# Optimization experiments

Measured on AMD Instinct MI355X. Metric: run time of the kernel, lower is better.

The kernel has to match this reference:

```python
import jax, jax.numpy as jnp
import numpy as np

NUM_HEADS = 16
NUM_KV_HEADS = 4
HEAD_DIM = 128
TOP_K = 4
RMS_EPS = 1e-6
ROPE_THETA = 10000.0


def setup_inputs() -> dict:
    key = jax.random.key(0)
    ks = jax.random.split(key, 10)
    T, h, E, I, SI = 1024, 2048, 16, 512, 1024
    s = 0.02  # weight init scale for numerical sanity
    return {
        "hidden_states": jax.random.normal(ks[0], (T, h), jnp.float32),
        "residual": jax.random.normal(ks[1], (T, h), jnp.float32),
        "rms1_w": jnp.ones((h,), jnp.float32),
        "rms2_w": jnp.ones((h,), jnp.float32),
        "w_qkv": jax.random.normal(ks[2], (h, NUM_HEADS * HEAD_DIM + 2 * NUM_KV_HEADS * HEAD_DIM), jnp.float32) * s,
        "w_dense": jax.random.normal(ks[3], (NUM_HEADS * HEAD_DIM, h), jnp.float32) * s,
        "gate_w": jax.random.normal(ks[4], (h, E), jnp.float32) * s,
        "w13": jax.random.normal(ks[5], (E, h, 2 * I), jnp.float32) * s,
        "w2": jax.random.normal(ks[6], (E, I, h), jnp.float32) * s,
        "sw13": jax.random.normal(ks[7], (h, 2 * SI), jnp.float32) * s,
        "sw2": jax.random.normal(ks[8], (SI, h), jnp.float32) * s,
        "position_ids": jnp.arange(T, dtype=jnp.int32),
    }


def _rmsnorm(x, w, eps=RMS_EPS):
    var = jnp.mean(jnp.square(x), axis=-1, keepdims=True)
    return x * jax.lax.rsqrt(var + eps) * w


def _rope_neox(pos, x):
    # x: [T, H, D]; rotate-half (neox) style over full head_dim
    d = x.shape[-1]
    inv_freq = 1.0 / (ROPE_THETA ** (jnp.arange(0, d, 2, dtype=jnp.float32) / d))  # [d/2]
    ang = pos.astype(jnp.float32)[:, None] * inv_freq  # [T, d/2]
    cos = jnp.cos(ang)[:, None, :]  # [T, 1, d/2]
    sin = jnp.sin(ang)[:, None, :]
    x1, x2 = x[..., : d // 2], x[..., d // 2 :]
    return jnp.concatenate([x1 * cos - x2 * sin, x2 * cos + x1 * sin], axis=-1)


def reference(hidden_states, residual, rms1_w, rms2_w, w_qkv, w_dense,
              gate_w, w13, w2, sw13, sw2, position_ids):
    T, h = hidden_states.shape
    q_size = NUM_HEADS * HEAD_DIM
    kv_size = NUM_KV_HEADS * HEAD_DIM

    # --- input RMSNorm with fused residual add ---
    resid = hidden_states + residual
    x = _rmsnorm(resid, rms1_w)

    # --- attention ---
    qkv = x @ w_qkv
    q = qkv[:, :q_size].reshape(T, NUM_HEADS, HEAD_DIM)
    k = qkv[:, q_size : q_size + kv_size].reshape(T, NUM_KV_HEADS, HEAD_DIM)
    v = qkv[:, q_size + kv_size :].reshape(T, NUM_KV_HEADS, HEAD_DIM)
    q = _rope_neox(position_ids, q)
    k = _rope_neox(position_ids, k)
    rep = NUM_HEADS // NUM_KV_HEADS
    kr = jnp.repeat(k, rep, axis=1)  # [T, H, D]
    vr = jnp.repeat(v, rep, axis=1)
    scale = HEAD_DIM ** -0.5
    scores = jnp.einsum('thd,shd->hts', q, kr) * scale  # [H, T, T]
    causal = jnp.tril(jnp.ones((T, T), dtype=bool))
    scores = jnp.where(causal[None], scores, -1e9)
    probs = jax.nn.softmax(scores, axis=-1)
    ctx = jnp.einsum('hts,shd->thd', probs, vr).reshape(T, q_size)
    attn_out = ctx @ w_dense

    # --- post-attention RMSNorm with fused residual add ---
    resid2 = attn_out + resid
    x2 = _rmsnorm(resid2, rms2_w)

    # --- shared experts (SiLU-and-mul MLP) ---
    gu = x2 @ sw13
    sg, su = jnp.split(gu, 2, axis=-1)
    shared = (jax.nn.silu(sg) * su) @ sw2

    # --- MoE routing: softmax -> top-k -> renormalize ---
    E = gate_w.shape[1]
    router_probs = jax.nn.softmax(x2 @ gate_w, axis=-1)  # [T, E]
    topk_w, topk_ids = jax.lax.top_k(router_probs, TOP_K)
    topk_w = topk_w / jnp.sum(topk_w, axis=-1, keepdims=True)
    comb = jnp.zeros((T, E), x2.dtype).at[jnp.arange(T)[:, None], topk_ids].add(topk_w)

    # --- experts (dense grouped-GEMM equivalent, combined by routing weights) ---
    h_all = jnp.einsum('td,edf->etf', x2, w13)  # [E, T, 2I]
    eg, eu = jnp.split(h_all, 2, axis=-1)
    act = jax.nn.silu(eg) * eu  # [E, T, I]
    moe = jnp.einsum('etf,efh,te->th', act, w2, comb)

    return (moe + shared, resid2)
```

## Files before the change

### kernel.cpp

```cpp
#include <hip/hip_runtime.h>
#include <math.h>

#define HD 2048
#define NQH 16
#define NKVH 4
#define HEADD 128
#define QKVN 3072
#define NEXP 16
#define EI 512
#define SSI 1024
#define TOPK 4
#define TT 1024

typedef __bf16 bf16x8 __attribute__((ext_vector_type(8)));
typedef float f32x4 __attribute__((ext_vector_type(4)));

static __device__ __forceinline__ unsigned short f2bf(float f) {
    union { float f; unsigned int u; } v; v.f = f;
    unsigned int r = v.u + 0x7fff + ((v.u >> 16) & 1);
    return (unsigned short)(r >> 16);
}

static __device__ __forceinline__ void gl_lds16(const unsigned short* g,
                                                unsigned short* l) {
    __builtin_amdgcn_global_load_lds(
        (const __attribute__((address_space(1))) unsigned int*)g,
        (__attribute__((address_space(3))) unsigned int*)l, 16, 0, 0);
}

__global__ __launch_bounds__(256) void add_rmsnorm_kernel(
    const float* __restrict__ a, const float* __restrict__ b,
    const float* __restrict__ w, float* __restrict__ resid_out,
    unsigned short* __restrict__ x_bf)
{
    int t = blockIdx.x;
    int tid = threadIdx.x;
    const float4* a4 = (const float4*)(a + (size_t)t * HD);
    const float4* b4 = b ? (const float4*)(b + (size_t)t * HD) : nullptr;
    float4* r4 = resid_out ? (float4*)(resid_out + (size_t)t * HD) : nullptr;
    const float4* w4 = (const float4*)w;

    float4 v[2];
    float ss = 0.f;
#pragma unroll
    for (int l = 0; l < 2; ++l) {
        int idx = tid + l * 256;
        float4 va = a4[idx];
        if (b4) {
            float4 vb = b4[idx];
            va.x += vb.x; va.y += vb.y; va.z += vb.z; va.w += vb.w;
        }
        if (r4) r4[idx] = va;
        v[l] = va;
        ss += va.x * va.x + va.y * va.y + va.z * va.z + va.w * va.w;
    }
    for (int off = 32; off > 0; off >>= 1) ss += __shfl_down(ss, off);
    __shared__ float red[4];
    int lane = tid & 63, wv = tid >> 6;
    if (lane == 0) red[wv] = ss;
    __syncthreads();
    if (tid == 0) {
        float s = red[0] + red[1] + red[2] + red[3];
        red[0] = rsqrtf(s / (float)HD + 1e-6f);
    }
    __syncthreads();
    float inv = red[0];
#pragma unroll
    for (int l = 0; l < 2; ++l) {
        int idx = tid + l * 256;
        float4 va = v[l], vw = w4[idx];
        ushort4 ob;
        ob.x = f2bf(va.x * inv * vw.x);
        ob.y = f2bf(va.y * inv * vw.y);
        ob.z = f2bf(va.z * inv * vw.z);
        ob.w = f2bf(va.w * inv * vw.w);
        ((ushort4*)(x_bf + (size_t)t * HD))[idx] = ob;
    }
}

__global__ __launch_bounds__(256) void transpose_convert(
    const float* __restrict__ in, unsigned short* __restrict__ out,
    int K, int N, long long strideIn, long long strideOut)
{
    __shared__ float tile[32][33];
    const int n0 = blockIdx.x * 32;
    const int k0 = blockIdx.y * 32;
    const float* ip = in + (size_t)blockIdx.z * strideIn;
    unsigned short* op = out + (size_t)blockIdx.z * strideOut;
    int tid = threadIdx.x;
    int r = tid >> 3, c = (tid & 7) * 4;
    float4 v = *(const float4*)(ip + (size_t)(k0 + r) * N + n0 + c);
    tile[r][c] = v.x; tile[r][c + 1] = v.y; tile[r][c + 2] = v.z; tile[r][c + 3] = v.w;
    __syncthreads();
    ushort4 o;
    o.x = f2bf(tile[c + 0][r]);
    o.y = f2bf(tile[c + 1][r]);
    o.z = f2bf(tile[c + 2][r]);
    o.w = f2bf(tile[c + 3][r]);
    *(ushort4*)(op + (size_t)(n0 + r) * K + k0 + c) = o;
}

#define SBK 64

__global__ __launch_bounds__(256) void gemm_splitk(
    const unsigned short* __restrict__ A, const unsigned short* __restrict__ B,
    float* __restrict__ Cpart, int M, int N, int Kc, int ldA, int ldB)
{
    __shared__ unsigned short As[2][128 * SBK];
    __shared__ unsigned short Bs[2][128 * SBK];

    const int tid = threadIdx.x;
    const int wave = tid >> 6;
    const int lane = tid & 63;
    const int wr = wave >> 1, wc = wave & 1;
    const int l15 = lane & 15;
    const int row0 = blockIdx.y * 128;
    const int col0 = blockIdx.x * 128;
    const int z = blockIdx.z;

    const unsigned short* Ap = A + (size_t)row0 * ldA + (size_t)z * Kc;
    const unsigned short* Bp = B + (size_t)col0 * ldB + (size_t)z * Kc;

    const int r_st = tid >> 3;
    const int q_st = tid & 7;
    const int csrc = (q_st ^ (r_st & 7)) << 3;

    f32x4 acc[4][4] = {};

    const int nsteps = Kc / SBK;

#define STAGE_SK(buf, k0s)                                                    \
    {                                                                         \
        _Pragma("unroll")                                                     \
        for (int i = 0; i < 4; ++i) {                                         \
            int rr = r_st + i * 32;                                           \
            gl_lds16(Ap + (size_t)rr * ldA + (k0s) + csrc,                    \
                     &As[buf][rr * SBK + q_st * 8]);                          \
            gl_lds16(Bp + (size_t)rr * ldB + (k0s) + csrc,                    \
                     &Bs[buf][rr * SBK + q_st * 8]);                          \
        }                                                                     \
    }

    STAGE_SK(0, 0);
    __syncthreads();

    for (int s = 0; s < nsteps; ++s) {
        const int cur = s & 1;
        if (s + 1 < nsteps) STAGE_SK(cur ^ 1, (s + 1) * SBK);

#pragma unroll
        for (int half = 0; half < 2; ++half) {
            const int q = half * 4 + (lane >> 4);
            bf16x8 af[4], bfv[4];
#pragma unroll
            for (int i = 0; i < 4; ++i) {
                int R = wr * 64 + i * 16 + l15;
                af[i] = *(const bf16x8*)&As[cur][R * SBK + ((q ^ (R & 7)) << 3)];
            }
#pragma unroll
            for (int j = 0; j < 4; ++j) {
                int R = wc * 64 + j * 16 + l15;
                bfv[j] = *(const bf16x8*)&Bs[cur][R * SBK + ((q ^ (R & 7)) << 3)];
            }
#pragma unroll
            for (int mi = 0; mi < 4; ++mi)
#pragma unroll
                for (int nj = 0; nj < 4; ++nj)
                    acc[mi][nj] = __builtin_amdgcn_mfma_f32_16x16x32_bf16(
                        af[mi], bfv[nj], acc[mi][nj], 0, 0, 0);
        }
        __syncthreads();
    }

    float* Cp = Cpart + (size_t)z * M * N;
#pragma unroll
    for (int mi = 0; mi < 4; ++mi)
#pragma unroll
        for (int nj = 0; nj < 4; ++nj)
#pragma unroll
            for (int r = 0; r < 4; ++r) {
                int row = row0 + wr * 64 + mi * 16 + (lane >> 4) * 4 + r;
                int col = col0 + wc * 64 + nj * 16 + l15;
                Cp[(size_t)row * N + col] = acc[mi][nj][r];
            }
}

__global__ __launch_bounds__(256) void reduce_partials(
    const float* __restrict__ part, int ns, int n4,
    const float* __restrict__ add, float* __restrict__ out, int acc)
{
    const float4* p4 = (const float4*)part;
    const float4* a4 = (const float4*)add;
    float4* o4 = (float4*)out;
    for (int idx = blockIdx.x * 256 + threadIdx.x; idx < n4;
         idx += gridDim.x * 256) {
        float4 s = p4[idx];
        for (int z = 1; z < ns; ++z) {
            float4 q = p4[(size_t)z * n4 + idx];
            s.x += q.x; s.y += q.y; s.z += q.z; s.w += q.w;
        }
        if (add) {
            float4 q = a4[idx];
            s.x += q.x; s.y += q.y; s.z += q.z; s.w += q.w;
        }
        if (acc) {
            float4 q = o4[idx];
            s.x += q.x; s.y += q.y; s.z += q.z; s.w += q.w;
        }
        o4[idx] = s;
    }
}

__global__ __launch_bounds__(256) void reduce_swiglu(
    const float* __restrict__ part, int ns, unsigned short* __restrict__ out)
{
    int idx4 = blockIdx.x * 256 + threadIdx.x;
    int t = idx4 >> 8;
    int i4 = (idx4 & 255) * 4;
    const float4* pg = (const float4*)(part + (size_t)t * (2 * SSI) + i4);
    const float4* pu = (const float4*)(part + (size_t)t * (2 * SSI) + SSI + i4);
    float4 g = pg[0], u = pu[0];
    for (int z = 1; z < ns; ++z) {
        float4 g2 = *(const float4*)((const float*)pg + (size_t)z * TT * 2 * SSI);
        float4 u2 = *(const float4*)((const float*)pu + (size_t)z * TT * 2 * SSI);
        g.x += g2.x; g.y += g2.y; g.z += g2.z; g.w += g2.w;
        u.x += u2.x; u.y += u2.y; u.z += u2.z; u.w += u2.w;
    }
    ushort4 o;
    o.x = f2bf((g.x / (1.f + __expf(-g.x))) * u.x);
    o.y = f2bf((g.y / (1.f + __expf(-g.y))) * u.y);
    o.z = f2bf((g.z / (1.f + __expf(-g.z))) * u.z);
    o.w = f2bf((g.w / (1.f + __expf(-g.w))) * u.w);
    *(ushort4*)(out + (size_t)t * SSI + i4) = o;
}

__global__ __launch_bounds__(256) void build_lists(
    const float* __restrict__ comb, int* __restrict__ lists,
    int* __restrict__ cnts)
{
    int e = blockIdx.x;
    int tid = threadIdx.x;
    __shared__ int sc[256];
    int loc[4];
    int c = 0;
#pragma unroll
    for (int j = 0; j < 4; ++j) {
        int t = tid * 4 + j;
        if (comb[(size_t)t * NEXP + e] > 0.f) loc[c++] = t;
    }
    sc[tid] = c;
    __syncthreads();
    for (int off = 1; off < 256; off <<= 1) {
        int v = (tid >= off) ? sc[tid - off] : 0;
        __syncthreads();
        sc[tid] += v;
        __syncthreads();
    }
    int base = sc[tid] - c;
    for (int i = 0; i < c; ++i) lists[e * TT + base + i] = loc[i];
    if (tid == 255) cnts[e] = sc[255];
}

__global__ __launch_bounds__(256) void moe_up_gather(
    const unsigned short* __restrict__ x2B,
    const unsigned short* __restrict__ w13T,
    const float* __restrict__ comb,
    const int* __restrict__ lists,
    const int* __restrict__ cnts,
    unsigned short* __restrict__ actB)
{
    __shared__ unsigned short As[2][64 * 32];
    __shared__ unsigned short Bgs[2][128 * 32];
    __shared__ unsigned short Bus[2][128 * 32];

    const int e = blockIdx.z;
    const int cnt = cnts[e];
    const int m0 = blockIdx.y * 64;
    if (m0 >= cnt) return;
    const int n0 = blockIdx.x * 128;

    const int tid = threadIdx.x;
    const int w = tid >> 6;
    const int lane = tid & 63;
    const int l15 = lane & 15;
    const int g = lane >> 4;

    const int r_st = tid >> 2;
    const int q_st = tid & 3;
    const int swz = (q_st ^ (r_st & 3)) << 3;

    int arow = m0 + r_st;
    int atok = lists[e * TT + (arow < cnt ? arow : cnt - 1)];
    const unsigned short* Asrc = x2B + (size_t)atok * HD;
    const unsigned short* Bbase = w13T + (size_t)e * 1024 * HD;

    f32x4 ag[4][2] = {};
    f32x4 au[4][2] = {};

#define STAGE_UP(buf, k0s)                                                    \
    {                                                                         \
        gl_lds16(Asrc + (k0s) + swz, &As[buf][r_st * 32 + q_st * 8]);         \
        _Pragma("unroll")                                                     \
        for (int i = 0; i < 2; ++i) {                                         \
            int rr = r_st + i * 64;                                           \
            gl_lds16(Bbase + (size_t)(n0 + rr) * HD + (k0s) + swz,            \
                     &Bgs[buf][rr * 32 + q_st * 8]);                          \
            gl_lds16(Bbase + (size_t)(512 + n0 + rr) * HD + (k0s) + swz,      \
                     &Bus[buf][rr * 32 + q_st * 8]);                          \
        }                                                                     \
    }

    STAGE_UP(0, 0);
    __syncthreads();

    const int nsteps = HD / 32;
    for (int s = 0; s < nsteps; ++s) {
        const int cur = s & 1;
        if (s + 1 < nsteps) STAGE_UP(cur ^ 1, (s + 1) * 32);

        bf16x8 af[4], bg[2], bu[2];
#pragma unroll
        for (int i = 0; i < 4; ++i) {
            int R = i * 16 + l15;
            af[i] = *(const bf16x8*)&As[cur][R * 32 + ((g ^ (R & 3)) << 3)];
        }
#pragma unroll
        for (int j = 0; j < 2; ++j) {
            int R = w * 32 + j * 16 + l15;
            int off = R * 32 + ((g ^ (R & 3)) << 3);
            bg[j] = *(const bf16x8*)&Bgs[cur][off];
            bu[j] = *(const bf16x8*)&Bus[cur][off];
        }
#pragma unroll
        for (int mi = 0; mi < 4; ++mi)
#pragma unroll
            for (int nj = 0; nj < 2; ++nj) {
                ag[mi][nj] = __builtin_amdgcn_mfma_f32_16x16x32_bf16(
                    af[mi], bg[nj], ag[mi][nj], 0, 0, 0);
                au[mi][nj] = __builtin_amdgcn_mfma_f32_16x16x32_bf16(
                    af[mi], bu[nj], au[mi][nj], 0, 0, 0);
            }
        __syncthreads();
    }

#pragma unroll
    for (int mi = 0; mi < 4; ++mi) {
#pragma unroll
        for (int r = 0; r < 4; ++r) {
            int grow = m0 + mi * 16 + g * 4 + r;
            if (grow >= cnt) continue;
            int tok = lists[e * TT + grow];
            float cw = comb[(size_t)tok * NEXP + e];
#pragma unroll
            for (int nj = 0; nj < 2; ++nj) {
                int col = n0 + w * 32 + nj * 16 + l15;
                float gg = ag[mi][nj][r];
                float uu = au[mi][nj][r];
                float v = (gg / (1.f + __expf(-gg))) * uu * cw;
                actB[(size_t)tok * (NEXP * EI) + e * EI + col] = f2bf(v);
            }
        }
    }
}

__global__ __launch_bounds__(256) void rope_pack(
    const float* __restrict__ qkv, const int* __restrict__ pos_ids,
    unsigned short* __restrict__ Qb, unsigned short* __restrict__ Kb,
    unsigned short* __restrict__ Vb)
{
    const float SCALE = 0.08838834764831843f;
    int t = blockIdx.x;
    int tid = threadIdx.x;
    int w = tid >> 6, lane = tid & 63;
    float pos = (float)pos_ids[t];
    float invf = powf(10000.0f, -(float)lane * (1.0f / 64.0f));
    float ang = pos * invf;
    float c = cosf(ang);
    float s = sinf(ang);
    const float* row = qkv + (size_t)t * QKVN;
#pragma unroll
    for (int j = 0; j < 5; ++j) {
        int hh = w * 5 + j;
        const float* hb = row + hh * HEADD;
        float x1 = hb[lane], x2 = hb[lane + 64];
        float o1 = x1 * c - x2 * s;
        float o2 = x2 * c + x1 * s;
        if (hh < NQH) {
            unsigned short* qp = Qb + ((size_t)hh * TT + t) * HEADD;
            qp[lane] = f2bf(o1 * SCALE);
            qp[lane + 64] = f2bf(o2 * SCALE);
        } else {
            unsigned short* kp = Kb + ((size_t)(hh - NQH) * TT + t) * HEADD;
            kp[lane] = f2bf(o1);
            kp[lane + 64] = f2bf(o2);
        }
    }
    float2 v2 = *(const float2*)(row + 2560 + tid * 2);
    int kvh = tid >> 6;
    int d = (tid * 2) & 127;
    unsigned int packed = (unsigned int)f2bf(v2.x) |
                          ((unsigned int)f2bf(v2.y) << 16);
    *(unsigned int*)(Vb + ((size_t)kvh * TT + t) * HEADD + d) = packed;
}

__global__ __launch_bounds__(256) void transpose_v(
    const unsigned short* __restrict__ Vb, unsigned short* __restrict__ Vt)
{
    __shared__ unsigned short tile[32][40];
    const int kvh = blockIdx.z;
    const int t0 = blockIdx.x * 32, d0 = blockIdx.y * 32;
    int tid = threadIdx.x;
    int r = tid >> 3, c4 = (tid & 7) * 4;
    ushort4 v = *(const ushort4*)(Vb + ((size_t)kvh * TT + t0 + r) * HEADD + d0 + c4);
    tile[r][c4] = v.x; tile[r][c4 + 1] = v.y;
    tile[r][c4 + 2] = v.z; tile[r][c4 + 3] = v.w;
    __syncthreads();
    ushort4 o;
    o.x = tile[c4 + 0][r];
    o.y = tile[c4 + 1][r];
    o.z = tile[c4 + 2][r];
    o.w = tile[c4 + 3][r];
    *(ushort4*)(Vt + ((size_t)kvh * HEADD + d0 + r) * TT + t0 + c4) = o;
}

__global__ __launch_bounds__(128) void flash_attn_mfma(
    const unsigned short* __restrict__ Qb,
    const unsigned short* __restrict__ Kb,
    const unsigned short* __restrict__ Vt,
    unsigned short* __restrict__ ctx)
{
    __shared__ __align__(16) unsigned short Ks[2][64 * 128];
    __shared__ __align__(16) unsigned short Vs[2][128 * 64];
    __shared__ __align__(16) unsigned short Pl[2][16][72];

    const int h   = blockIdx.x;
    const int p   = blockIdx.y;
    const int rh  = blockIdx.z;
    const int kvh = h >> 2;
    const int tid = threadIdx.x;
    const int w   = tid >> 6;
    const int lane = tid & 63;
    const int l15 = lane & 15;
    const int g   = lane >> 4;

    const int krow = tid >> 4;
    const int kch  = tid & 15;
    const int vch  = tid & 7;

    const unsigned short* Kh = Kb + (size_t)kvh * TT * HEADD;
    const unsigned short* Vh = Vt + (size_t)kvh * HEADD * TT;

#define STAGE_KV(buf, s0s)                                                    \
    {                                                                         \
        _Pragma("unroll")                                                     \
        for (int i = 0; i < 8; ++i) {                                         \
            int idx = tid + i * 128;                                          \
            int r = idx >> 4, c = idx & 15;                                   \
            int csw = (c & 8) | ((c ^ r) & 7);                                \
            gl_lds16(Kh + (size_t)((s0s) + r) * HEADD + csw * 8,              \
                     &Ks[buf][idx * 8]);                                      \
        }                                                                     \
        _Pragma("unroll")                                                     \
        for (int i = 0; i < 8; ++i) {                                         \
            int idx = tid + i * 128;                                          \
            int r = idx >> 3, c = idx & 7;                                    \
            int csw = (c ^ r) & 7;                                            \
            gl_lds16(Vh + (size_t)r * TT + (s0s) + csw * 8,                   \
                     &Vs[buf][idx * 8]);                                      \
        }                                                                     \
    }

    const int qts[2] = {p, 15 - p};

#pragma unroll
    for (int qi = 0; qi < 2; ++qi) {
        const int qt = qts[qi];
        const int q0 = qt * 64 + rh * 32 + w * 16;
        const int ntiles = qt + 1;

        const unsigned short* Qrow = Qb + ((size_t)h * TT + q0 + l15) * HEADD;
        bf16x8 qf[4];
#pragma unroll
        for (int kk = 0; kk < 4; ++kk)
            qf[kk] = *(const bf16x8*)(Qrow + kk * 32 + g * 8);

        float m_i[4], l_i[4];
#pragma unroll
        for (int r = 0; r < 4; ++r) { m_i[r] = -1e30f; l_i[r] = 0.f; }
        f32x4 of[8] = {};

        STAGE_KV(0, 0);
        __syncthreads();

        for (int st = 0; st < ntiles; ++st) {
            const int cur = st & 1;
            const int s0 = st * 64;
            if (st + 1 < ntiles) STAGE_KV(cur ^ 1, (st + 1) * 64);

            f32x4 sacc[4] = {};
#pragma unroll
            for (int kk = 0; kk < 4; ++kk) {
#pragma unroll
                for (int n = 0; n < 4; ++n) {
                    int R = n * 16 + l15;
                    int cidx = kk * 4 + g;
                    int cs = (cidx & 8) | ((cidx ^ R) & 7);
                    bf16x8 kb = *(const bf16x8*)&Ks[cur][R * 128 + cs * 8];
                    sacc[n] = __builtin_amdgcn_mfma_f32_16x16x32_bf16(
                        qf[kk], kb, sacc[n], 0, 0, 0);
                }
            }

            const bool diag = (st == qt);
            float alpha[4];
#pragma unroll
            for (int r = 0; r < 4; ++r) {
                const int qrow = q0 + g * 4 + r;
                float sv[4] = {sacc[0][r], sacc[1][r], sacc[2][r], sacc[3][r]};
                if (diag) {
#pragma unroll
                    for (int n = 0; n < 4; ++n)
                        if (s0 + n * 16 + l15 > qrow) sv[n] = -1e30f;
                }
                float rm = fmaxf(fmaxf(sv[0], sv[1]), fmaxf(sv[2], sv[3]));
                rm = fmaxf(rm, __shfl_xor(rm, 1));
                rm = fmaxf(rm, __shfl_xor(rm, 2));
                rm = fmaxf(rm, __shfl_xor(rm, 4));
                rm = fmaxf(rm, __shfl_xor(rm, 8));
                float mnew = fmaxf(m_i[r], rm);
                alpha[r] = __expf(m_i[r] - mnew);
                float p0 = __expf(sv[0] - mnew);
                float p1 = __expf(sv[1] - mnew);
                float p2 = __expf(sv[2] - mnew);
                float p3 = __expf(sv[3] - mnew);
                float rs = p0 + p1 + p2 + p3;
                rs += __shfl_xor(rs, 1);
                rs += __shfl_xor(rs, 2);
                rs += __shfl_xor(rs, 4);
                rs += __shfl_xor(rs, 8);
                l_i[r] = l_i[r] * alpha[r] + rs;
                m_i[r] = mnew;
                Pl[w][g * 4 + r][0 * 16 + l15] = f2bf(p0);
                Pl[w][g * 4 + r][1 * 16 + l15] = f2bf(p1);
                Pl[w][g * 4 + r][2 * 16 + l15] = f2bf(p2);
                Pl[w][g * 4 + r][3 * 16 + l15] = f2bf(p3);
            }

#pragma unroll
            for (int nd = 0; nd < 8; ++nd)
#pragma unroll
                for (int r = 0; r < 4; ++r)
                    of[nd][r] *= alpha[r];

#pragma unroll
            for (int kk2 = 0; kk2 < 2; ++kk2) {
                bf16x8 pa = *(const bf16x8*)&Pl[w][l15][kk2 * 32 + g * 8];
#pragma unroll
                for (int nd = 0; nd < 8; ++nd) {
                    int R = nd * 16 + l15;
                    int cidx = kk2 * 4 + g;
                    int cs = (cidx ^ R) & 7;
                    bf16x8 vb = *(const bf16x8*)&Vs[cur][R * 64 + cs * 8];
                    of[nd] = __builtin_amdgcn_mfma_f32_16x16x32_bf16(
                        pa, vb, of[nd], 0, 0, 0);
                }
            }
            __syncthreads();
        }

        float invl[4];
#pragma unroll
        for (int r = 0; r < 4; ++r) invl[r] = 1.f / l_i[r];
#pragma unroll
        for (int nd = 0; nd < 8; ++nd)
#pragma unroll
            for (int r = 0; r < 4; ++r) {
                int trow = q0 + g * 4 + r;
                ctx[(size_t)trow * (NQH * HEADD) + h * HEADD + nd * 16 + l15] =
                    f2bf(of[nd][r] * invl[r]);
            }
    }
}

__global__ __launch_bounds__(256) void router_fused(
    const float* __restrict__ resid2, const float* __restrict__ w,
    const float* __restrict__ gate_w, float* __restrict__ comb)
{
    int t = blockIdx.x;
    int tid = threadIdx.x;
    int lane = tid & 63, wv = tid >> 6;

    const float4* r4 = (const float4*)(resid2 + (size_t)t * HD);
    float4 xa = r4[tid * 2], xb = r4[tid * 2 + 1];
    float ss = xa.x * xa.x + xa.y * xa.y + xa.z * xa.z + xa.w * xa.w +
               xb.x * xb.x + xb.y * xb.y + xb.z * xb.z + xb.w * xb.w;
    for (int off = 32; off > 0; off >>= 1) ss += __shfl_down(ss, off);
    __shared__ float red[4];
    if (lane == 0) red[wv] = ss;
    __syncthreads();
    float inv = rsqrtf((red[0] + red[1] + red[2] + red[3]) / (float)HD + 1e-6f);

    const float4* w4 = (const float4*)w;
    float4 wa = w4[tid * 2], wb = w4[tid * 2 + 1];
    float xs[8] = {xa.x * wa.x * inv, xa.y * wa.y * inv, xa.z * wa.z * inv,
                   xa.w * wa.w * inv, xb.x * wb.x * inv, xb.y * wb.y * inv,
                   xb.z * wb.z * inv, xb.w * wb.w * inv};

    float acc[16] = {};
    int kbase = tid * 8;
#pragma unroll
    for (int j = 0; j < 8; ++j) {
        float xv = xs[j];
        const float4* wrow = (const float4*)(gate_w + (size_t)(kbase + j) * NEXP);
        float4 w0 = wrow[0], w1 = wrow[1], w2 = wrow[2], w3 = wrow[3];
        acc[0] += xv * w0.x;  acc[1] += xv * w0.y;  acc[2] += xv * w0.z;  acc[3] += xv * w0.w;
        acc[4] += xv * w1.x;  acc[5] += xv * w1.y;  acc[6] += xv * w1.z;  acc[7] += xv * w1.w;
        acc[8] += xv * w2.x;  acc[9] += xv * w2.y;  acc[10] += xv * w2.z; acc[11] += xv * w2.w;
        acc[12] += xv * w3.x; acc[13] += xv * w3.y; acc[14] += xv * w3.z; acc[15] += xv * w3.w;
    }
    __shared__ float red2[4][16];
#pragma unroll
    for (int e = 0; e < 16; ++e) {
        float v = acc[e];
        v += __shfl_xor(v, 1);
        v += __shfl_xor(v, 2);
        v += __shfl_xor(v, 4);
        v += __shfl_xor(v, 8);
        v += __shfl_xor(v, 16);
        v += __shfl_xor(v, 32);
        if (lane == 0) red2[wv][e] = v;
    }
    __syncthreads();

    if (tid == 0) {
        float l[NEXP];
#pragma unroll
        for (int e = 0; e < NEXP; ++e)
            l[e] = red2[0][e] + red2[1][e] + red2[2][e] + red2[3][e];
        int sel[TOPK];
        float selv[TOPK];
        bool used[NEXP] = {};
#pragma unroll
        for (int r = 0; r < TOPK; ++r) {
            int best = -1;
            float bv = -1e30f;
            for (int e = 0; e < NEXP; ++e)
                if (!used[e] && l[e] > bv) { bv = l[e]; best = e; }
            used[best] = true;
            sel[r] = best;
            selv[r] = bv;
        }
        float mx = selv[0];
        float wsum = 0.f, wvv[TOPK];
#pragma unroll
        for (int r = 0; r < TOPK; ++r) { wvv[r] = __expf(selv[r] - mx); wsum += wvv[r]; }
        float out16[NEXP] = {};
#pragma unroll
        for (int r = 0; r < TOPK; ++r) out16[sel[r]] = wvv[r] / wsum;
#pragma unroll
        for (int e = 0; e < NEXP; ++e) comb[(size_t)t * NEXP + e] = out16[e];
    }
}

extern "C" void kernel_launch(void* const* d_in, const int* in_sizes, int n_in,
                              void* d_out, int out_size, void* d_ws, size_t ws_size,
                              hipStream_t stream)
{
    const float* hidden   = (const float*)d_in[0];
    const float* residual = (const float*)d_in[1];
    const float* rms1_w   = (const float*)d_in[2];
    const float* rms2_w   = (const float*)d_in[3];
    const float* w_qkv    = (const float*)d_in[4];
    const float* w_dense  = (const float*)d_in[5];
    const float* gate_w   = (const float*)d_in[6];
    const float* w13      = (const float*)d_in[7];
    const float* w2       = (const float*)d_in[8];
    const float* sw13     = (const float*)d_in[9];
    const float* sw2      = (const float*)d_in[10];
    const int*   pos_ids  = (const int*)d_in[11];

    const int T = TT;

    float* out0 = (float*)d_out;
    float* out1 = (float*)d_out + (size_t)T * HD;

    char* base = (char*)d_ws;
    float*          residF = (float*)(base);
    unsigned short* xB     = (unsigned short*)(base + 8388608);
    unsigned short* ctxB   = (unsigned short*)(base + 12582912);
    unsigned short* actB   = (unsigned short*)(base);
    float*          qkvF   = (float*)(base + 16777216);
    unsigned short* x2B    = (unsigned short*)(base + 29360128);
    unsigned short* sactB  = (unsigned short*)(base + 33554432);
    float*          comb   = (float*)(base + 35651584);
    float*          part   = (float*)(base + 35717120);
    unsigned short* Wbuf   = (unsigned short*)(base + 69271552);
    int*            lists  = (int*)(base + 139526144);
    int*            cnts   = (int*)(base + 139591680);

    unsigned short* Qb = (unsigned short*)(base + 35717120);
    unsigned short* Kb = Qb + (size_t)NQH * TT * HEADD;
    unsigned short* Vb = Kb + (size_t)NKVH * TT * HEADD;
    unsigned short* Vt = Vb + (size_t)NKVH * TT * HEADD;

    dim3 blk(256);

    add_rmsnorm_kernel<<<dim3(T), blk, 0, stream>>>(
        hidden, residual, rms1_w, residF, xB);

    transpose_convert<<<dim3(QKVN / 32, HD / 32), blk, 0, stream>>>(
        w_qkv, Wbuf, HD, QKVN, 0, 0);
    gemm_splitk<<<dim3(QKVN / 128, T / 128, 2), blk, 0, stream>>>(
        xB, Wbuf, part, T, QKVN, 1024, HD, HD);
    reduce_partials<<<dim3(1024), blk, 0, stream>>>(
        part, 2, T * QKVN / 4, nullptr, qkvF, 0);

    rope_pack<<<dim3(T), blk, 0, stream>>>(qkvF, pos_ids, Qb, Kb, Vb);
    transpose_v<<<dim3(T / 32, HEADD / 32, NKVH), blk, 0, stream>>>(Vb, Vt);

    flash_attn_mfma<<<dim3(NQH, 8, 2), dim3(128), 0, stream>>>(Qb, Kb, Vt, ctxB);

    transpose_convert<<<dim3(HD / 32, HD / 32), blk, 0, stream>>>(
        w_dense, Wbuf, HD, HD, 0, 0);
    gemm_splitk<<<dim3(HD / 128, T / 128, 4), blk, 0, stream>>>(
        ctxB, Wbuf, part, T, HD, 512, HD, HD);
    reduce_partials<<<dim3(1024), blk, 0, stream>>>(
        part, 4, T * HD / 4, residF, out1, 0);

    add_rmsnorm_kernel<<<dim3(T), blk, 0, stream>>>(
        out1, nullptr, rms2_w, nullptr, x2B);

    router_fused<<<dim3(T), blk, 0, stream>>>(out1, rms2_w, gate_w, comb);
    build_lists<<<dim3(NEXP), blk, 0, stream>>>(comb, lists, cnts);

    transpose_convert<<<dim3(HD / 32, HD / 32), blk, 0, stream>>>(
        sw13, Wbuf, HD, 2 * SSI, 0, 0);
    gemm_splitk<<<dim3(HD / 128, T / 128, 4), blk, 0, stream>>>(
        x2B, Wbuf, part, T, 2 * SSI, 512, HD, HD);

    reduce_swiglu<<<dim3(T * SSI / 4 / 256), blk, 0, stream>>>(part, 4, sactB);

    transpose_convert<<<dim3(HD / 32, SSI / 32), blk, 0, stream>>>(
        sw2, Wbuf, SSI, HD, 0, 0);
    gemm_splitk<<<dim3(HD / 128, T / 128, 4), blk, 0, stream>>>(
        sactB, Wbuf, part, T, HD, 256, SSI, SSI);
    reduce_partials<<<dim3(1024), blk, 0, stream>>>(
        part, 4, T * HD / 4, nullptr, out0, 0);

    hipMemsetAsync(actB, 0, (size_t)T * NEXP * EI * 2, stream);
    transpose_convert<<<dim3(1024 / 32, HD / 32, NEXP), blk, 0, stream>>>(
        w13, Wbuf, HD, 1024, (long long)HD * 1024, (long long)1024 * HD);
    moe_up_gather<<<dim3(EI / 128, 16, NEXP), blk, 0, stream>>>(
        x2B, Wbuf, comb, lists, cnts, actB);

    transpose_convert<<<dim3(HD / 32, (NEXP * EI) / 32), blk, 0, stream>>>(
        w2, Wbuf, NEXP * EI, HD, 0, 0);
    gemm_splitk<<<dim3(HD / 128, T / 128, 4), blk, 0, stream>>>(
        actB, Wbuf, part, T, HD, 2048, NEXP * EI, NEXP * EI);
    reduce_partials<<<dim3(1024), blk, 0, stream>>>(
        part, 4, T * HD / 4, nullptr, out0, 1);
}
```

Baseline: 404.9 us.

## Replace dense MoE down GEMM with grouped gather GEMM over routed tokens

The MoE down projection used to be a dense split-K GEMM over all 16 experts' activations, most of them zero. It now runs a per-expert grouped GEMM over only the routed tokens, writing each result into one of four top-k slot partial buffers that the existing reduction sums. The up kernel writes compacted per-expert activations, so the memset of the large sparse activation buffer is dropped, and its tile shape moves to 64x64 with a 64-wide K step. This adds a per-token slot computation in build_lists and a tiny single-thread scan kernel. It also relies on every token filling exactly four slots, so any unused slot buffer would keep stale data.

```diff
diff --git a/kernel.cpp b/kernel.cpp
--- a/kernel.cpp
+++ b/kernel.cpp
@@ -236,7 +236,7 @@
 
 __global__ __launch_bounds__(256) void build_lists(
     const float* __restrict__ comb, int* __restrict__ lists,
-    int* __restrict__ cnts)
+    int* __restrict__ slots, int* __restrict__ cnts)
 {
     int e = blockIdx.x;
     int tid = threadIdx.x;
@@ -257,8 +257,24 @@
         __syncthreads();
     }
     int base = sc[tid] - c;
-    for (int i = 0; i < c; ++i) lists[e * TT + base + i] = loc[i];
+    for (int i = 0; i < c; ++i) {
+        int t = loc[i];
+        int s = 0;
+        for (int e2 = 0; e2 < e; ++e2)
+            s += (comb[(size_t)t * NEXP + e2] > 0.f) ? 1 : 0;
+        lists[e * TT + base + i] = t;
+        slots[e * TT + base + i] = s;
+    }
     if (tid == 255) cnts[e] = sc[255];
+}
+
+__global__ void scan_cnts(const int* __restrict__ cnts, int* __restrict__ bases)
+{
+    if (threadIdx.x == 0 && blockIdx.x == 0) {
+        int a = 0;
+        for (int e = 0; e < NEXP; ++e) { bases[e] = a; a += cnts[e]; }
+        bases[NEXP] = a;
+    }
 }
 
 __global__ __launch_bounds__(256) void moe_up_gather(
@@ -267,17 +283,123 @@
     const float* __restrict__ comb,
     const int* __restrict__ lists,
     const int* __restrict__ cnts,
-    unsigned short* __restrict__ actB)
-{
-    __shared__ unsigned short As[2][64 * 32];
-    __shared__ unsigned short Bgs[2][128 * 32];
-    __shared__ unsigned short Bus[2][128 * 32];
+    const int* __restrict__ bases,
+    unsigned short* __restrict__ actC)
+{
+    __shared__ unsigned short As[2][64 * 64];
+    __shared__ unsigned short Bgs[2][64 * 64];
+    __shared__ unsigned short Bus[2][64 * 64];
+
+    const int e = blockIdx.z;
+    const int cnt = cnts[e];
+    const int m0 = blockIdx.y * 64;
+    if (m0 >= cnt) return;
+    const int n0 = blockIdx.x * 64;
+    const int base_e = bases[e];
+
+    const int tid = threadIdx.x;
+    const int w = tid >> 6;
+    const int lane = tid & 63;
+    const int l15 = lane & 15;
+    const int g = lane >> 4;
+
+    const int r0 = tid >> 3;
+    const int q_st = tid & 7;
+    const int swz = (q_st ^ (r0 & 7)) << 3;
+
+    int a0 = m0 + r0, a1 = m0 + r0 + 32;
+    int tok0 = lists[e * TT + (a0 < cnt ? a0 : cnt - 1)];
+    int tok1 = lists[e * TT + (a1 < cnt ? a1 : cnt - 1)];
+    const unsigned short* Asrc0 = x2B + (size_t)tok0 * HD;
+    const unsigned short* Asrc1 = x2B + (size_t)tok1 * HD;
+    const unsigned short* Bbase = w13T + (size_t)e * 1024 * HD;
+    const unsigned short* Bg0 = Bbase + (size_t)(n0 + r0) * HD;
+    const unsigned short* Bg1 = Bbase + (size_t)(n0 + r0 + 32) * HD;
+    const unsigned short* Bu0 = Bg0 + (size_t)512 * HD;
+    const unsigned short* Bu1 = Bg1 + (size_t)512 * HD;
+
+    f32x4 ag[4] = {};
+    f32x4 au[4] = {};
+
+#define STAGE_UP(buf, k0s)                                                    \
+    {                                                                         \
+        gl_lds16(Asrc0 + (k0s) + swz, &As[buf][(tid) * 8]);                   \
+        gl_lds16(Asrc1 + (k0s) + swz, &As[buf][(tid + 256) * 8]);             \
+        gl_lds16(Bg0 + (k0s) + swz, &Bgs[buf][(tid) * 8]);                    \
+        gl_lds16(Bg1 + (k0s) + swz, &Bgs[buf][(tid + 256) * 8]);              \
+        gl_lds16(Bu0 + (k0s) + swz, &Bus[buf][(tid) * 8]);                    \
+        gl_lds16(Bu1 + (k0s) + swz, &Bus[buf][(tid + 256) * 8]);              \
+    }
+
+    STAGE_UP(0, 0);
+    __syncthreads();
+
+    const int nsteps = HD / 64;
+    for (int s = 0; s < nsteps; ++s) {
+        const int cur = s & 1;
+        if (s + 1 < nsteps) STAGE_UP(cur ^ 1, (s + 1) * 64);
+
+#pragma unroll
+        for (int kk2 = 0; kk2 < 2; ++kk2) {
+            const int q = kk2 * 4 + g;
+            bf16x8 af[4], bg, bu;
+#pragma unroll
+            for (int i = 0; i < 4; ++i) {
+                int R = i * 16 + l15;
+                af[i] = *(const bf16x8*)&As[cur][R * 64 + ((q ^ (R & 7)) << 3)];
+            }
+            {
+                int R = w * 16 + l15;
+                int off = R * 64 + ((q ^ (R & 7)) << 3);
+                bg = *(const bf16x8*)&Bgs[cur][off];
+                bu = *(const bf16x8*)&Bus[cur][off];
+            }
+#pragma unroll
+            for (int mi = 0; mi < 4; ++mi) {
+                ag[mi] = __builtin_amdgcn_mfma_f32_16x16x32_bf16(
+                    af[mi], bg, ag[mi], 0, 0, 0);
+                au[mi] = __builtin_amdgcn_mfma_f32_16x16x32_bf16(
+                    af[mi], bu, au[mi], 0, 0, 0);
+            }
+        }
+        __syncthreads();
+    }
+
+#pragma unroll
+    for (int mi = 0; mi < 4; ++mi) {
+#pragma unroll
+        for (int r = 0; r < 4; ++r) {
+            int grow = m0 + mi * 16 + g * 4 + r;
+            if (grow >= cnt) continue;
+            int tok = lists[e * TT + grow];
+            float cw = comb[(size_t)tok * NEXP + e];
+            int col = n0 + w * 16 + l15;
+            float gg = ag[mi][r];
+            float uu = au[mi][r];
+            float v = (gg / (1.f + __expf(-gg))) * uu * cw;
+            actC[(size_t)(base_e + grow) * EI + col] = f2bf(v);
+        }
+    }
+}
+
+__global__ __launch_bounds__(256) void moe_down_gather(
+    const unsigned short* __restrict__ actC,
+    const unsigned short* __restrict__ w2T,
+    const int* __restrict__ lists,
+    const int* __restrict__ slots,
+    const int* __restrict__ cnts,
+    const int* __restrict__ bases,
+    float* __restrict__ slotpart)
+{
+    __shared__ unsigned short As[2][64 * 64];
+    __shared__ unsigned short Bs[2][128 * 64];
 
     const int e = blockIdx.z;
     const int cnt = cnts[e];
     const int m0 = blockIdx.y * 64;
     if (m0 >= cnt) return;
     const int n0 = blockIdx.x * 128;
+    const int base_e = bases[e];
 
     const int tid = threadIdx.x;
     const int w = tid >> 6;
@@ -285,61 +407,60 @@
     const int l15 = lane & 15;
     const int g = lane >> 4;
 
-    const int r_st = tid >> 2;
-    const int q_st = tid & 3;
-    const int swz = (q_st ^ (r_st & 3)) << 3;
-
-    int arow = m0 + r_st;
-    int atok = lists[e * TT + (arow < cnt ? arow : cnt - 1)];
-    const unsigned short* Asrc = x2B + (size_t)atok * HD;
-    const unsigned short* Bbase = w13T + (size_t)e * 1024 * HD;
-
-    f32x4 ag[4][2] = {};
-    f32x4 au[4][2] = {};
-
-#define STAGE_UP(buf, k0s)                                                    \
+    const int r0 = tid >> 3;
+    const int q_st = tid & 7;
+    const int swz = (q_st ^ (r0 & 7)) << 3;
+
+    int a0 = m0 + r0, a1 = m0 + r0 + 32;
+    const unsigned short* Asrc0 =
+        actC + (size_t)(base_e + (a0 < cnt ? a0 : cnt - 1)) * EI;
+    const unsigned short* Asrc1 =
+        actC + (size_t)(base_e + (a1 < cnt ? a1 : cnt - 1)) * EI;
+    const unsigned short* Bbase = w2T + (size_t)e * EI;
+
+#define STAGE_DN(buf, k0s)                                                    \
     {                                                                         \
-        gl_lds16(Asrc + (k0s) + swz, &As[buf][r_st * 32 + q_st * 8]);         \
+        gl_lds16(Asrc0 + (k0s) + swz, &As[buf][(tid) * 8]);                   \
+        gl_lds16(Asrc1 + (k0s) + swz, &As[buf][(tid + 256) * 8]);             \
         _Pragma("unroll")                                                     \
-        for (int i = 0; i < 2; ++i) {                                         \
-            int rr = r_st + i * 64;                                           \
-            gl_lds16(Bbase + (size_t)(n0 + rr) * HD + (k0s) + swz,            \
-                     &Bgs[buf][rr * 32 + q_st * 8]);                          \
-            gl_lds16(Bbase + (size_t)(512 + n0 + rr) * HD + (k0s) + swz,      \
-                     &Bus[buf][rr * 32 + q_st * 8]);                          \
+        for (int i = 0; i < 4; ++i) {                                         \
+            int rr = r0 + i * 32;                                             \
+            gl_lds16(Bbase + (size_t)(n0 + rr) * (NEXP * EI) + (k0s) + swz,   \
+                     &Bs[buf][(tid + i * 256) * 8]);                          \
         }                                                                     \
     }
 
-    STAGE_UP(0, 0);
-    __syncthreads();
-
-    const int nsteps = HD / 32;
+    f32x4 acc[4][2] = {};
+
+    STAGE_DN(0, 0);
+    __syncthreads();
+
+    const int nsteps = EI / 64;
     for (int s = 0; s < nsteps; ++s) {
         const int cur = s & 1;
-        if (s + 1 < nsteps) STAGE_UP(cur ^ 1, (s + 1) * 32);
-
-        bf16x8 af[4], bg[2], bu[2];
-#pragma unroll
-        for (int i = 0; i < 4; ++i) {
-            int R = i * 16 + l15;
-            af[i] = *(const bf16x8*)&As[cur][R * 32 + ((g ^ (R & 3)) << 3)];
-        }
-#pragma unroll
-        for (int j = 0; j < 2; ++j) {
-            int R = w * 32 + j * 16 + l15;
-            int off = R * 32 + ((g ^ (R & 3)) << 3);
-            bg[j] = *(const bf16x8*)&Bgs[cur][off];
-            bu[j] = *(const bf16x8*)&Bus[cur][off];
-        }
-#pragma unroll
-        for (int mi = 0; mi < 4; ++mi)
-#pragma unroll
-            for (int nj = 0; nj < 2; ++nj) {
-                ag[mi][nj] = __builtin_amdgcn_mfma_f32_16x16x32_bf16(
-                    af[mi], bg[nj], ag[mi][nj], 0, 0, 0);
-                au[mi][nj] = __builtin_amdgcn_mfma_f32_16x16x32_bf16(
-                    af[mi], bu[nj], au[mi][nj], 0, 0, 0);
-            }
+        if (s + 1 < nsteps) STAGE_DN(cur ^ 1, (s + 1) * 64);
+
+#pragma unroll
+        for (int kk2 = 0; kk2 < 2; ++kk2) {
+            const int q = kk2 * 4 + g;
+            bf16x8 af[4], bf[2];
+#pragma unroll
+            for (int i = 0; i < 4; ++i) {
+                int R = i * 16 + l15;
+                af[i] = *(const bf16x8*)&As[cur][R * 64 + ((q ^ (R & 7)) << 3)];
+            }
+#pragma unroll
+            for (int j = 0; j < 2; ++j) {
+                int R = w * 32 + j * 16 + l15;
+                bf[j] = *(const bf16x8*)&Bs[cur][R * 64 + ((q ^ (R & 7)) << 3)];
+            }
+#pragma unroll
+            for (int mi = 0; mi < 4; ++mi)
+#pragma unroll
+                for (int nj = 0; nj < 2; ++nj)
+                    acc[mi][nj] = __builtin_amdgcn_mfma_f32_16x16x32_bf16(
+                        af[mi], bf[nj], acc[mi][nj], 0, 0, 0);
+        }
         __syncthreads();
     }
 
@@ -350,14 +471,12 @@
             int grow = m0 + mi * 16 + g * 4 + r;
             if (grow >= cnt) continue;
             int tok = lists[e * TT + grow];
-            float cw = comb[(size_t)tok * NEXP + e];
+            int sl  = slots[e * TT + grow];
+            float* orow = slotpart + (size_t)sl * TT * HD + (size_t)tok * HD;
 #pragma unroll
             for (int nj = 0; nj < 2; ++nj) {
                 int col = n0 + w * 32 + nj * 16 + l15;
-                float gg = ag[mi][nj][r];
-                float uu = au[mi][nj][r];
-                float v = (gg / (1.f + __expf(-gg))) * uu * cw;
-                actB[(size_t)tok * (NEXP * EI) + e * EI + col] = f2bf(v);
+                orow[col] = acc[mi][nj][r];
             }
         }
     }
@@ -442,10 +561,6 @@
     const int lane = tid & 63;
     const int l15 = lane & 15;
     const int g   = lane >> 4;
-
-    const int krow = tid >> 4;
-    const int kch  = tid & 15;
-    const int vch  = tid & 7;
 
     const unsigned short* Kh = Kb + (size_t)kvh * TT * HEADD;
     const unsigned short* Vh = Vt + (size_t)kvh * HEADD * TT;
@@ -688,7 +803,7 @@
     float*          residF = (float*)(base);
     unsigned short* xB     = (unsigned short*)(base + 8388608);
     unsigned short* ctxB   = (unsigned short*)(base + 12582912);
-    unsigned short* actB   = (unsigned short*)(base);
+    unsigned short* actC   = (unsigned short*)(base);
     float*          qkvF   = (float*)(base + 16777216);
     unsigned short* x2B    = (unsigned short*)(base + 29360128);
     unsigned short* sactB  = (unsigned short*)(base + 33554432);
@@ -697,6 +812,8 @@
     unsigned short* Wbuf   = (unsigned short*)(base + 69271552);
     int*            lists  = (int*)(base + 139526144);
     int*            cnts   = (int*)(base + 139591680);
+    int*            slots  = (int*)(base + 139591936);
+    int*            bases  = (int*)(base + 139657472);
 
     unsigned short* Qb = (unsigned short*)(base + 35717120);
     unsigned short* Kb = Qb + (size_t)NQH * TT * HEADD;
@@ -731,7 +848,8 @@
         out1, nullptr, rms2_w, nullptr, x2B);
 
     router_fused<<<dim3(T), blk, 0, stream>>>(out1, rms2_w, gate_w, comb);
-    build_lists<<<dim3(NEXP), blk, 0, stream>>>(comb, lists, cnts);
+    build_lists<<<dim3(NEXP), blk, 0, stream>>>(comb, lists, slots, cnts);
+    scan_cnts<<<dim3(1), dim3(64), 0, stream>>>(cnts, bases);
 
     transpose_convert<<<dim3(HD / 32, HD / 32), blk, 0, stream>>>(
         sw13, Wbuf, HD, 2 * SSI, 0, 0);
@@ -747,16 +865,15 @@
     reduce_partials<<<dim3(1024), blk, 0, stream>>>(
         part, 4, T * HD / 4, nullptr, out0, 0);
 
-    hipMemsetAsync(actB, 0, (size_t)T * NEXP * EI * 2, stream);
     transpose_convert<<<dim3(1024 / 32, HD / 32, NEXP), blk, 0, stream>>>(
         w13, Wbuf, HD, 1024, (long long)HD * 1024, (long long)1024 * HD);
-    moe_up_gather<<<dim3(EI / 128, 16, NEXP), blk, 0, stream>>>(
-        x2B, Wbuf, comb, lists, cnts, actB);
+    moe_up_gather<<<dim3(EI / 64, 16, NEXP), blk, 0, stream>>>(
+        x2B, Wbuf, comb, lists, cnts, bases, actC);
 
     transpose_convert<<<dim3(HD / 32, (NEXP * EI) / 32), blk, 0, stream>>>(
         w2, Wbuf, NEXP * EI, HD, 0, 0);
-    gemm_splitk<<<dim3(HD / 128, T / 128, 4), blk, 0, stream>>>(
-        actB, Wbuf, part, T, HD, 2048, NEXP * EI, NEXP * EI);
+    moe_down_gather<<<dim3(HD / 128, 16, NEXP), blk, 0, stream>>>(
+        actC, Wbuf, lists, slots, cnts, bases, part);
     reduce_partials<<<dim3(1024), blk, 0, stream>>>(
         part, 4, T * HD / 4, nullptr, out0, 1);
 }
```

Result: faster. 380.1 us (-6.1%).
